# Optimization experiments

Hardware: AMD Instinct MI355X
Metric: run time of the kernel (lower is better)

The kernel has to match this reference:

```python
import jax, jax.numpy as jnp
import numpy as np

N = 100_000      # nodes
E = 3_200_000    # edges (avg degree 32)
F = 16           # irrep feature channels
IR = 4           # (max_l+1)**2 with max_l = 1
DENOM = 32.0     # denominator init kwarg
EPS = 1e-9
INV_S3 = 1.0 / np.sqrt(3.0).astype(np.float32)  # CG norm for 1x1->0
INV_S2 = 1.0 / np.sqrt(2.0).astype(np.float32)  # CG norm for 1x1->1


def setup_inputs() -> dict:
    key = jax.random.key(0)
    k0, k1, k2, k3, k4 = jax.random.split(key, 5)
    positions = jax.random.normal(k0, (N, 3), jnp.float32)
    node_feats = jax.random.normal(k1, (N, F, IR), jnp.float32)
    W = jax.random.normal(k2, (IR, IR), jnp.float32) / np.float32(np.sqrt(IR))
    b = jnp.zeros((IR,), jnp.float32)
    senders = jax.random.randint(k3, (E,), 0, N)
    receivers = jax.random.randint(k4, (E,), 0, N)
    return dict(positions=positions, node_feats=node_feats, W=W, b=b,
                senders=senders, receivers=receivers)


def reference(positions, node_feats, W, b, senders, receivers):
    # --- edge update: SH of normalized relative position, CG tensor product ---
    d = positions[receivers] - positions[senders]               # [E, 3]
    d = d / (jnp.linalg.norm(d, axis=-1, keepdims=True) + EPS)  # unit direction
    # real spherical harmonics up to l=1: sh0 = 1, sh1 = unit direction
    sh1 = d[:, None, :]                                         # [E, 1, 3]

    x = node_feats[senders]                                     # [E, F, 4]
    x0 = x[..., 0:1]                                            # l=0 part [E,F,1]
    x1 = x[..., 1:4]                                            # l=1 part [E,F,3]

    # CG paths with l3 <= max_l = 1:
    #   0x0->0 (identity), 1x1->0 (dot / sqrt3)
    out0 = x0 + jnp.sum(x1 * sh1, axis=-1, keepdims=True) * INV_S3      # [E,F,1]
    #   0x1->1, 1x0->1 (identities), 1x1->1 (cross / sqrt2)
    cross = jnp.cross(x1, jnp.broadcast_to(sh1, x1.shape))
    out1 = x0 * sh1 + x1 + cross * INV_S2                               # [E,F,3]
    tp = jnp.concatenate([out0, out1], axis=-1)                         # [E,F,4]

    # --- node update: segment-sum over receivers, scale, Dense over coeff dim ---
    agg = jax.ops.segment_sum(tp, receivers, num_segments=positions.shape[0])
    agg = agg / DENOM                                                   # [N,F,4]
    return agg @ W + b                                                  # [N,F,4]
```

## Files before the change

### kernel.cpp

```cpp
#include <hip/hip_runtime.h>
#include <hip/hip_fp16.h>


#define F_DIM 16
#define BIN_SHIFT 6
#define BIN_NODES (1 << BIN_SHIFT)
#define HALF_NODES (BIN_NODES / 2)
#define CHUNK 8192
#define CAP_LDS 1408
#define MAXBINS 2048

__global__ void __launch_bounds__(256) pack_kernel(
    const float* __restrict__ pos, const float* __restrict__ nf,
    float4* __restrict__ posf4, uint2* __restrict__ nfh,
    int* __restrict__ binCur, int N, int nbins, int cap)
{
    int tid = blockIdx.x * blockDim.x + threadIdx.x;
    int total = N * F_DIM;
    if (tid < total) {
        float4 q = ((const float4*)nf)[tid];
        __half2 h01 = __floats2half2_rn(q.x, q.y);
        __half2 h23 = __floats2half2_rn(q.z, q.w);
        uint2 u;
        u.x = *reinterpret_cast<unsigned*>(&h01);
        u.y = *reinterpret_cast<unsigned*>(&h23);
        nfh[tid] = u;
    }
    if (tid < N)
        posf4[tid] = make_float4(pos[3*tid], pos[3*tid+1], pos[3*tid+2], 0.f);
    if (tid < nbins)
        binCur[tid] = tid * cap;
}

__global__ void __launch_bounds__(512) build_bins_kernel(
    const int* __restrict__ senders, const int* __restrict__ receivers,
    int* __restrict__ binCur, int* __restrict__ bins,
    int nbins, int cap, int E)
{
    __shared__ int hbase[MAXBINS];
    __shared__ int hrank[MAXBINS];
    int t = threadIdx.x;
    for (int i = t; i < nbins; i += 512) { hbase[i] = 0; hrank[i] = 0; }
    __syncthreads();

    int base = blockIdx.x * CHUNK;
    int end  = base + CHUNK; if (end > E) end = E;

    for (int e = base + t; e < end; e += 512)
        atomicAdd(&hbase[((unsigned)receivers[e]) >> BIN_SHIFT], 1);
    __syncthreads();

    for (int i = t; i < nbins; i += 512) {
        int c = hbase[i];
        hbase[i] = (c > 0) ? atomicAdd(&binCur[i], c) : 0;
    }
    __syncthreads();

    for (int e = base + t; e < end; e += 512) {
        int r = receivers[e];
        int s = senders[e];
        int bb = r >> BIN_SHIFT;
        int rank = atomicAdd(&hrank[bb], 1);
        int dest = hbase[bb] + rank;
        if (dest < (bb + 1) * cap)
            bins[dest] = (s << BIN_SHIFT) | (r & (BIN_NODES - 1));
    }
}

__device__ __forceinline__ float4 unpack_h4(uint2 u)
{
    __half2 h01 = *reinterpret_cast<__half2*>(&u.x);
    __half2 h23 = *reinterpret_cast<__half2*>(&u.y);
    float2 a = __half22float2(h01);
    float2 b = __half22float2(h23);
    return make_float4(a.x, a.y, b.x, b.y);
}

__device__ __forceinline__ void edge_acc_d(
    float dx, float dy, float dz, const float4& fx,
    float& a0, float& a1, float& a2, float& a3)
{
    const float INV_S3 = 0.5773502691896258f;
    const float INV_S2 = 0.7071067811865476f;
    float dot = fx.y*dx + fx.z*dy + fx.w*dz;
    a0 += fx.x + dot * INV_S3;
    float c0 = fx.z*dz - fx.w*dy;
    float c1 = fx.w*dx - fx.y*dz;
    float c2 = fx.y*dy - fx.z*dx;
    a1 += fx.x*dx + fx.y + c0 * INV_S2;
    a2 += fx.x*dy + fx.z + c1 * INV_S2;
    a3 += fx.x*dz + fx.w + c2 * INV_S2;
}

__global__ void __launch_bounds__(256) bin_gather_kernel(
    const float4* __restrict__ posf4,
    const uint2* __restrict__ nfh,
    const int* __restrict__ bins,
    const int* __restrict__ binCur,
    const float* __restrict__ W,
    const float* __restrict__ Bias,
    float* __restrict__ out,
    int N, int cap)
{
    __shared__ float4 ledge[CAP_LDS];
    __shared__ int lhist[HALF_NODES];
    __shared__ int lscan[HALF_NODES];
    __shared__ int lstart[HALF_NODES];

    int t = threadIdx.x;
    int bin  = blockIdx.x >> 1;
    int half = blockIdx.x & 1;
    int node0 = (bin << BIN_SHIFT) + half * HALF_NODES;
    int gbase = bin * cap;

    int cnt = binCur[bin] - gbase;
    if (cnt > cap) cnt = cap;

    if (t < HALF_NODES) lhist[t] = 0;
    __syncthreads();

    for (int j = t; j < cnt; j += 256) {
        int rl = bins[gbase + j] & (BIN_NODES - 1);
        if ((rl >> 5) == half) atomicAdd(&lhist[rl & (HALF_NODES - 1)], 1);
    }
    __syncthreads();

    if (t < HALF_NODES) lscan[t] = lhist[t];
    __syncthreads();
    for (int off = 1; off < HALF_NODES; off <<= 1) {
        int v = (t < HALF_NODES && t >= off) ? lscan[t - off] : 0;
        __syncthreads();
        if (t < HALF_NODES) lscan[t] += v;
        __syncthreads();
    }
    if (t < HALF_NODES) { lstart[t] = lscan[t] - lhist[t]; lhist[t] = 0; }
    __syncthreads();

    for (int j = t; j < cnt; j += 256) {
        int pk = bins[gbase + j];
        int rl = pk & (BIN_NODES - 1);
        if ((rl >> 5) != half) continue;
        int rl32 = rl & (HALF_NODES - 1);
        int s = pk >> BIN_SHIFT;
        int rank = atomicAdd(&lhist[rl32], 1);
        int dest = lstart[rl32] + rank;
        if (dest >= CAP_LDS) continue;
        float4 ps = posf4[s];
        float4 pr = posf4[node0 + rl32];
        float dx = pr.x - ps.x;
        float dy = pr.y - ps.y;
        float dz = pr.z - ps.z;
        float d2 = dx*dx + dy*dy + dz*dz;
        float inv = __builtin_amdgcn_rsqf(fmaxf(d2, 1e-18f));
        float4 rec;
        rec.x = dx * inv;
        rec.y = dy * inv;
        rec.z = dz * inv;
        rec.w = __int_as_float(s);
        ledge[dest] = rec;
    }
    __syncthreads();

    float w[16];
#pragma unroll
    for (int i = 0; i < 16; ++i) w[i] = W[i];
    float b0 = Bias[0], b1 = Bias[1], b2 = Bias[2], b3 = Bias[3];
    const float sc = 1.0f / 32.0f;

    int f = t & 15;

    for (int nl = t >> 4; nl < HALF_NODES; nl += 16) {
        int n = node0 + nl;
        if (n >= N) break;
        int s0 = lstart[nl];
        int dcnt = lscan[nl] - s0;
        if (dcnt > CAP_LDS - s0) dcnt = CAP_LDS - s0;

        float a0 = 0.f, a1 = 0.f, a2 = 0.f, a3 = 0.f;
        int j = 0;
        for (; j + 4 <= dcnt; j += 4) {
            float4 e0 = ledge[s0 + j + 0];
            float4 e1 = ledge[s0 + j + 1];
            float4 e2 = ledge[s0 + j + 2];
            float4 e3 = ledge[s0 + j + 3];
            int s_0 = __float_as_int(e0.w);
            int s_1 = __float_as_int(e1.w);
            int s_2 = __float_as_int(e2.w);
            int s_3 = __float_as_int(e3.w);
            uint2 u0 = nfh[(unsigned)(s_0 * F_DIM + f)];
            uint2 u1 = nfh[(unsigned)(s_1 * F_DIM + f)];
            uint2 u2 = nfh[(unsigned)(s_2 * F_DIM + f)];
            uint2 u3 = nfh[(unsigned)(s_3 * F_DIM + f)];
            edge_acc_d(e0.x, e0.y, e0.z, unpack_h4(u0), a0, a1, a2, a3);
            edge_acc_d(e1.x, e1.y, e1.z, unpack_h4(u1), a0, a1, a2, a3);
            edge_acc_d(e2.x, e2.y, e2.z, unpack_h4(u2), a0, a1, a2, a3);
            edge_acc_d(e3.x, e3.y, e3.z, unpack_h4(u3), a0, a1, a2, a3);
        }
        for (; j < dcnt; ++j) {
            float4 e0 = ledge[s0 + j];
            int s = __float_as_int(e0.w);
            uint2 u = nfh[(unsigned)(s * F_DIM + f)];
            edge_acc_d(e0.x, e0.y, e0.z, unpack_h4(u), a0, a1, a2, a3);
        }

        a0 *= sc; a1 *= sc; a2 *= sc; a3 *= sc;
        float4 o;
        o.x = a0*w[0] + a1*w[4] + a2*w[8]  + a3*w[12] + b0;
        o.y = a0*w[1] + a1*w[5] + a2*w[9]  + a3*w[13] + b1;
        o.z = a0*w[2] + a1*w[6] + a2*w[10] + a3*w[14] + b2;
        o.w = a0*w[3] + a1*w[7] + a2*w[11] + a3*w[15] + b3;
        ((float4*)out)[(size_t)n * F_DIM + f] = o;
    }
}

__global__ void __launch_bounds__(256) hist_kernel(
    const int* __restrict__ receivers, int* __restrict__ deg,
    int* __restrict__ rank, int E)
{
    int e = blockIdx.x * blockDim.x + threadIdx.x;
    if (e >= E) return;
    rank[e] = atomicAdd(&deg[receivers[e]], 1);
}

__global__ void __launch_bounds__(256) alloc_kernel(
    const int* __restrict__ deg, int* __restrict__ start,
    int* __restrict__ cursor, int N)
{
    __shared__ int tmp[256];
    __shared__ int base;
    int t = threadIdx.x;
    int n = blockIdx.x * blockDim.x + t;
    int v = (n < N) ? deg[n] : 0;
    tmp[t] = v;
    __syncthreads();
    for (int off = 1; off < 256; off <<= 1) {
        int x = (t >= off) ? tmp[t - off] : 0;
        __syncthreads();
        tmp[t] += x;
        __syncthreads();
    }
    int incl = tmp[t];
    if (t == 255) base = atomicAdd(cursor, incl);
    __syncthreads();
    if (n < N) start[n] = base + incl - v;
}

__global__ void __launch_bounds__(256) scatter_kernel(
    const int* __restrict__ senders, const int* __restrict__ receivers,
    const int* __restrict__ rank, const int* __restrict__ start,
    int* __restrict__ csr_s, int E)
{
    int e = blockIdx.x * blockDim.x + threadIdx.x;
    if (e >= E) return;
    csr_s[start[receivers[e]] + rank[e]] = senders[e];
}

__global__ void __launch_bounds__(256) gather_kernel(
    const float* __restrict__ pos,
    const float* __restrict__ nf,
    const int* __restrict__ csr_s,
    const int* __restrict__ start,
    const int* __restrict__ deg,
    const float* __restrict__ W,
    const float* __restrict__ b,
    float* __restrict__ out,
    int N)
{
    const float INV_S3 = 0.5773502691896258f;
    const float INV_S2 = 0.7071067811865476f;

    int tid = blockIdx.x * blockDim.x + threadIdx.x;
    int n = tid >> 4;
    if (n >= N) return;
    int f = tid & 15;

    float rx = pos[3*n], ry = pos[3*n+1], rz = pos[3*n+2];
    int s0 = start[n];
    int dcnt = deg[n];
    float a0 = 0.f, a1 = 0.f, a2 = 0.f, a3 = 0.f;
    const float4* nf4 = (const float4*)nf;

    for (int j = 0; j < dcnt; ++j) {
        int s = csr_s[s0 + j];
        float dx = rx - pos[3*s], dy = ry - pos[3*s+1], dz = rz - pos[3*s+2];
        float d2 = dx*dx + dy*dy + dz*dz;
        float inv = __builtin_amdgcn_rsqf(fmaxf(d2, 1e-18f));
        dx *= inv; dy *= inv; dz *= inv;
        float4 x = nf4[(unsigned)(s * F_DIM + f)];
        float dot = x.y*dx + x.z*dy + x.w*dz;
        a0 += x.x + dot * INV_S3;
        float c0 = x.z*dz - x.w*dy, c1 = x.w*dx - x.y*dz, c2 = x.y*dy - x.z*dx;
        a1 += x.x*dx + x.y + c0 * INV_S2;
        a2 += x.x*dy + x.z + c1 * INV_S2;
        a3 += x.x*dz + x.w + c2 * INV_S2;
    }
    const float sc = 1.0f / 32.0f;
    a0 *= sc; a1 *= sc; a2 *= sc; a3 *= sc;
    float4 o;
    o.x = a0*W[0] + a1*W[4] + a2*W[8]  + a3*W[12] + b[0];
    o.y = a0*W[1] + a1*W[5] + a2*W[9]  + a3*W[13] + b[1];
    o.z = a0*W[2] + a1*W[6] + a2*W[10] + a3*W[14] + b[2];
    o.w = a0*W[3] + a1*W[7] + a2*W[11] + a3*W[15] + b[3];
    ((float4*)out)[tid] = o;
}

extern "C" void kernel_launch(void* const* d_in, const int* in_sizes, int n_in,
                              void* d_out, int out_size, void* d_ws, size_t ws_size,
                              hipStream_t stream)
{
    const float* pos       = (const float*)d_in[0];
    const float* nf        = (const float*)d_in[1];
    const float* W         = (const float*)d_in[2];
    const float* b         = (const float*)d_in[3];
    const int*   senders   = (const int*)d_in[4];
    const int*   receivers = (const int*)d_in[5];

    int N = in_sizes[0] / 3;
    int E = in_sizes[4];
    float* out = (float*)d_out;
    const int blk = 256;

    int nbins = (N + BIN_NODES - 1) >> BIN_SHIFT;
    int cap   = E / nbins + 453;
    size_t need = (size_t)N * 16 + (size_t)N * F_DIM * 8
                + ((size_t)nbins + (size_t)nbins * cap) * 4;

    if (nbins <= MAXBINS && ws_size >= need) {
        float4* posf4 = (float4*)d_ws;
        uint2*  nfh   = (uint2*)(posf4 + N);
        int* binCur = (int*)(nfh + (size_t)N * F_DIM);
        int* bins   = binCur + nbins;

        int total = N * F_DIM;
        pack_kernel<<<(total + blk - 1) / blk, blk, 0, stream>>>(
            pos, nf, posf4, nfh, binCur, N, nbins, cap);
        build_bins_kernel<<<(E + CHUNK - 1) / CHUNK, 512, 0, stream>>>(
            senders, receivers, binCur, bins, nbins, cap, E);
        bin_gather_kernel<<<nbins * 2, blk, 0, stream>>>(
            posf4, nfh, bins, binCur, W, b, out, N, cap);
    } else {
        int* cursor = (int*)d_ws;
        int* deg    = cursor + 1;
        int* start  = deg + N;
        int* rank   = start + N;
        int* csr_s  = rank + E;

        hipMemsetAsync(cursor, 0, (size_t)(1 + N) * sizeof(int), stream);
        hist_kernel<<<(E + blk - 1) / blk, blk, 0, stream>>>(receivers, deg, rank, E);
        alloc_kernel<<<(N + blk - 1) / blk, blk, 0, stream>>>(deg, start, cursor, N);
        scatter_kernel<<<(E + blk - 1) / blk, blk, 0, stream>>>(
            senders, receivers, rank, start, csr_s, E);
        long total = (long)N * F_DIM;
        gather_kernel<<<(unsigned)((total + blk - 1) / blk), blk, 0, stream>>>(
            pos, nf, csr_s, start, deg, W, b, out, N);
    }
}
```

Measured before the change: 239.7 us.

## Fuse feature packing into bin-building kernel and halve edge chunk size

Merges the separate pack kernel (fp16 conversion of node features, float4 positions) into the bin-building kernel with grid-stride loops, and replaces the bin-cursor initialisation with a memset so bin counters start at zero and are offset per bin. The chunk size drops from 8192 to 4096 edges and the block size from 512 to 256 threads, giving about twice as many blocks for the binning pass. This removes one kernel launch and its tail, at the cost of an added memset and more global atomics on bin counters from the larger block count.

```diff
diff --git a/kernel.cpp b/kernel.cpp
--- a/kernel.cpp
+++ b/kernel.cpp
@@ -6,66 +6,9 @@
 #define BIN_SHIFT 6
 #define BIN_NODES (1 << BIN_SHIFT)
 #define HALF_NODES (BIN_NODES / 2)
-#define CHUNK 8192
+#define CHUNK 4096
 #define CAP_LDS 1408
 #define MAXBINS 2048
-
-__global__ void __launch_bounds__(256) pack_kernel(
-    const float* __restrict__ pos, const float* __restrict__ nf,
-    float4* __restrict__ posf4, uint2* __restrict__ nfh,
-    int* __restrict__ binCur, int N, int nbins, int cap)
-{
-    int tid = blockIdx.x * blockDim.x + threadIdx.x;
-    int total = N * F_DIM;
-    if (tid < total) {
-        float4 q = ((const float4*)nf)[tid];
-        __half2 h01 = __floats2half2_rn(q.x, q.y);
-        __half2 h23 = __floats2half2_rn(q.z, q.w);
-        uint2 u;
-        u.x = *reinterpret_cast<unsigned*>(&h01);
-        u.y = *reinterpret_cast<unsigned*>(&h23);
-        nfh[tid] = u;
-    }
-    if (tid < N)
-        posf4[tid] = make_float4(pos[3*tid], pos[3*tid+1], pos[3*tid+2], 0.f);
-    if (tid < nbins)
-        binCur[tid] = tid * cap;
-}
-
-__global__ void __launch_bounds__(512) build_bins_kernel(
-    const int* __restrict__ senders, const int* __restrict__ receivers,
-    int* __restrict__ binCur, int* __restrict__ bins,
-    int nbins, int cap, int E)
-{
-    __shared__ int hbase[MAXBINS];
-    __shared__ int hrank[MAXBINS];
-    int t = threadIdx.x;
-    for (int i = t; i < nbins; i += 512) { hbase[i] = 0; hrank[i] = 0; }
-    __syncthreads();
-
-    int base = blockIdx.x * CHUNK;
-    int end  = base + CHUNK; if (end > E) end = E;
-
-    for (int e = base + t; e < end; e += 512)
-        atomicAdd(&hbase[((unsigned)receivers[e]) >> BIN_SHIFT], 1);
-    __syncthreads();
-
-    for (int i = t; i < nbins; i += 512) {
-        int c = hbase[i];
-        hbase[i] = (c > 0) ? atomicAdd(&binCur[i], c) : 0;
-    }
-    __syncthreads();
-
-    for (int e = base + t; e < end; e += 512) {
-        int r = receivers[e];
-        int s = senders[e];
-        int bb = r >> BIN_SHIFT;
-        int rank = atomicAdd(&hrank[bb], 1);
-        int dest = hbase[bb] + rank;
-        if (dest < (bb + 1) * cap)
-            bins[dest] = (s << BIN_SHIFT) | (r & (BIN_NODES - 1));
-    }
-}
 
 __device__ __forceinline__ float4 unpack_h4(uint2 u)
 {
@@ -92,6 +35,59 @@
     a3 += fx.x*dz + fx.w + c2 * INV_S2;
 }
 
+__global__ void __launch_bounds__(256) build_pack_kernel(
+    const float* __restrict__ pos, const float* __restrict__ nf,
+    const int* __restrict__ senders, const int* __restrict__ receivers,
+    float4* __restrict__ posf4, uint2* __restrict__ nfh,
+    int* __restrict__ binCur, int* __restrict__ bins,
+    int N, int E, int nbins, int cap)
+{
+    __shared__ int hbase[MAXBINS];
+    __shared__ int hrank[MAXBINS];
+    int t = threadIdx.x;
+    for (int i = t; i < nbins; i += 256) { hbase[i] = 0; hrank[i] = 0; }
+
+    int gtid = blockIdx.x * 256 + t;
+    int gstride = gridDim.x * 256;
+    int total = N * F_DIM;
+    for (int i = gtid; i < total; i += gstride) {
+        float4 q = ((const float4*)nf)[i];
+        __half2 h01 = __floats2half2_rn(q.x, q.y);
+        __half2 h23 = __floats2half2_rn(q.z, q.w);
+        uint2 u;
+        u.x = *reinterpret_cast<unsigned*>(&h01);
+        u.y = *reinterpret_cast<unsigned*>(&h23);
+        nfh[i] = u;
+    }
+    for (int i = gtid; i < N; i += gstride)
+        posf4[i] = make_float4(pos[3*i], pos[3*i+1], pos[3*i+2], 0.f);
+    __syncthreads();
+
+    int base = blockIdx.x * CHUNK;
+    int end  = base + CHUNK; if (end > E) end = E;
+    if (base >= end) return;
+
+    for (int e = base + t; e < end; e += 256)
+        atomicAdd(&hbase[((unsigned)receivers[e]) >> BIN_SHIFT], 1);
+    __syncthreads();
+
+    for (int i = t; i < nbins; i += 256) {
+        int c = hbase[i];
+        hbase[i] = (c > 0) ? atomicAdd(&binCur[i], c) : 0;
+    }
+    __syncthreads();
+
+    for (int e = base + t; e < end; e += 256) {
+        int r = receivers[e];
+        int s = senders[e];
+        int bb = r >> BIN_SHIFT;
+        int rank = atomicAdd(&hrank[bb], 1);
+        int dest = hbase[bb] + rank;
+        if (dest < cap)
+            bins[(size_t)bb * cap + dest] = (s << BIN_SHIFT) | (r & (BIN_NODES - 1));
+    }
+}
+
 __global__ void __launch_bounds__(256) bin_gather_kernel(
     const float4* __restrict__ posf4,
     const uint2* __restrict__ nfh,
@@ -113,7 +109,7 @@
     int node0 = (bin << BIN_SHIFT) + half * HALF_NODES;
     int gbase = bin * cap;
 
-    int cnt = binCur[bin] - gbase;
+    int cnt = binCur[bin];
     if (cnt > cap) cnt = cap;
 
     if (t < HALF_NODES) lhist[t] = 0;
@@ -331,11 +327,10 @@
         int* binCur = (int*)(nfh + (size_t)N * F_DIM);
         int* bins   = binCur + nbins;
 
-        int total = N * F_DIM;
-        pack_kernel<<<(total + blk - 1) / blk, blk, 0, stream>>>(
-            pos, nf, posf4, nfh, binCur, N, nbins, cap);
-        build_bins_kernel<<<(E + CHUNK - 1) / CHUNK, 512, 0, stream>>>(
-            senders, receivers, binCur, bins, nbins, cap, E);
+        hipMemsetAsync(binCur, 0, (size_t)nbins * sizeof(int), stream);
+        build_pack_kernel<<<(E + CHUNK - 1) / CHUNK, blk, 0, stream>>>(
+            pos, nf, senders, receivers, posf4, nfh, binCur, bins,
+            N, E, nbins, cap);
         bin_gather_kernel<<<nbins * 2, blk, 0, stream>>>(
             posf4, nfh, bins, binCur, W, b, out, N, cap);
     } else {
```

Measured after the change: 266.7 us. +11.2%, slower.

## Replace LDS-histogram binning with direct global atomics on padded bin counters

Applied to the files above, without the earlier changes.

Drops the two-pass block-local histogram and per-block reservation in the edge binning kernel. Instead, every edge does one global atomicAdd on a per-bin counter, with counters padded to 16 ints apart to avoid false sharing, and writes straight to its slot. This removes two LDS passes, the block syncs and the double read of receivers. The cost is 3.2M global atomics contending on about 1563 counters, and the order of edges within a bin is no longer deterministic.

```diff
diff --git a/kernel.cpp b/kernel.cpp
--- a/kernel.cpp
+++ b/kernel.cpp
@@ -6,14 +6,39 @@
 #define BIN_SHIFT 6
 #define BIN_NODES (1 << BIN_SHIFT)
 #define HALF_NODES (BIN_NODES / 2)
-#define CHUNK 8192
 #define CAP_LDS 1408
 #define MAXBINS 2048
+#define CUR_STRIDE 16
+
+__device__ __forceinline__ float4 unpack_h4(uint2 u)
+{
+    __half2 h01 = *reinterpret_cast<__half2*>(&u.x);
+    __half2 h23 = *reinterpret_cast<__half2*>(&u.y);
+    float2 a = __half22float2(h01);
+    float2 b = __half22float2(h23);
+    return make_float4(a.x, a.y, b.x, b.y);
+}
+
+__device__ __forceinline__ void edge_acc_d(
+    float dx, float dy, float dz, const float4& fx,
+    float& a0, float& a1, float& a2, float& a3)
+{
+    const float INV_S3 = 0.5773502691896258f;
+    const float INV_S2 = 0.7071067811865476f;
+    float dot = fx.y*dx + fx.z*dy + fx.w*dz;
+    a0 += fx.x + dot * INV_S3;
+    float c0 = fx.z*dz - fx.w*dy;
+    float c1 = fx.w*dx - fx.y*dz;
+    float c2 = fx.y*dy - fx.z*dx;
+    a1 += fx.x*dx + fx.y + c0 * INV_S2;
+    a2 += fx.x*dy + fx.z + c1 * INV_S2;
+    a3 += fx.x*dz + fx.w + c2 * INV_S2;
+}
 
 __global__ void __launch_bounds__(256) pack_kernel(
     const float* __restrict__ pos, const float* __restrict__ nf,
     float4* __restrict__ posf4, uint2* __restrict__ nfh,
-    int* __restrict__ binCur, int N, int nbins, int cap)
+    int* __restrict__ binCur, int N, int nbins)
 {
     int tid = blockIdx.x * blockDim.x + threadIdx.x;
     int total = N * F_DIM;
@@ -28,68 +53,25 @@
     }
     if (tid < N)
         posf4[tid] = make_float4(pos[3*tid], pos[3*tid+1], pos[3*tid+2], 0.f);
-    if (tid < nbins)
-        binCur[tid] = tid * cap;
-}
-
-__global__ void __launch_bounds__(512) build_bins_kernel(
+    if (tid < nbins * CUR_STRIDE)
+        binCur[tid] = 0;
+}
+
+__global__ void __launch_bounds__(256) build_kernel(
     const int* __restrict__ senders, const int* __restrict__ receivers,
     int* __restrict__ binCur, int* __restrict__ bins,
-    int nbins, int cap, int E)
-{
-    __shared__ int hbase[MAXBINS];
-    __shared__ int hrank[MAXBINS];
-    int t = threadIdx.x;
-    for (int i = t; i < nbins; i += 512) { hbase[i] = 0; hrank[i] = 0; }
-    __syncthreads();
-
-    int base = blockIdx.x * CHUNK;
-    int end  = base + CHUNK; if (end > E) end = E;
-
-    for (int e = base + t; e < end; e += 512)
-        atomicAdd(&hbase[((unsigned)receivers[e]) >> BIN_SHIFT], 1);
-    __syncthreads();
-
-    for (int i = t; i < nbins; i += 512) {
-        int c = hbase[i];
-        hbase[i] = (c > 0) ? atomicAdd(&binCur[i], c) : 0;
-    }
-    __syncthreads();
-
-    for (int e = base + t; e < end; e += 512) {
+    int cap, int E)
+{
+    int gtid = blockIdx.x * 256 + threadIdx.x;
+    int gstride = gridDim.x * 256;
+    for (int e = gtid; e < E; e += gstride) {
         int r = receivers[e];
         int s = senders[e];
         int bb = r >> BIN_SHIFT;
-        int rank = atomicAdd(&hrank[bb], 1);
-        int dest = hbase[bb] + rank;
-        if (dest < (bb + 1) * cap)
-            bins[dest] = (s << BIN_SHIFT) | (r & (BIN_NODES - 1));
-    }
-}
-
-__device__ __forceinline__ float4 unpack_h4(uint2 u)
-{
-    __half2 h01 = *reinterpret_cast<__half2*>(&u.x);
-    __half2 h23 = *reinterpret_cast<__half2*>(&u.y);
-    float2 a = __half22float2(h01);
-    float2 b = __half22float2(h23);
-    return make_float4(a.x, a.y, b.x, b.y);
-}
-
-__device__ __forceinline__ void edge_acc_d(
-    float dx, float dy, float dz, const float4& fx,
-    float& a0, float& a1, float& a2, float& a3)
-{
-    const float INV_S3 = 0.5773502691896258f;
-    const float INV_S2 = 0.7071067811865476f;
-    float dot = fx.y*dx + fx.z*dy + fx.w*dz;
-    a0 += fx.x + dot * INV_S3;
-    float c0 = fx.z*dz - fx.w*dy;
-    float c1 = fx.w*dx - fx.y*dz;
-    float c2 = fx.y*dy - fx.z*dx;
-    a1 += fx.x*dx + fx.y + c0 * INV_S2;
-    a2 += fx.x*dy + fx.z + c1 * INV_S2;
-    a3 += fx.x*dz + fx.w + c2 * INV_S2;
+        int rank = atomicAdd(&binCur[bb * CUR_STRIDE], 1);
+        if (rank < cap)
+            bins[(size_t)bb * cap + rank] = (s << BIN_SHIFT) | (r & (BIN_NODES - 1));
+    }
 }
 
 __global__ void __launch_bounds__(256) bin_gather_kernel(
@@ -113,7 +95,7 @@
     int node0 = (bin << BIN_SHIFT) + half * HALF_NODES;
     int gbase = bin * cap;
 
-    int cnt = binCur[bin] - gbase;
+    int cnt = binCur[bin * CUR_STRIDE];
     if (cnt > cap) cnt = cap;
 
     if (t < HALF_NODES) lhist[t] = 0;
@@ -323,19 +305,19 @@
     int nbins = (N + BIN_NODES - 1) >> BIN_SHIFT;
     int cap   = E / nbins + 453;
     size_t need = (size_t)N * 16 + (size_t)N * F_DIM * 8
-                + ((size_t)nbins + (size_t)nbins * cap) * 4;
+                + ((size_t)nbins * CUR_STRIDE + (size_t)nbins * cap) * 4;
 
     if (nbins <= MAXBINS && ws_size >= need) {
         float4* posf4 = (float4*)d_ws;
         uint2*  nfh   = (uint2*)(posf4 + N);
         int* binCur = (int*)(nfh + (size_t)N * F_DIM);
-        int* bins   = binCur + nbins;
+        int* bins   = binCur + (size_t)nbins * CUR_STRIDE;
 
         int total = N * F_DIM;
         pack_kernel<<<(total + blk - 1) / blk, blk, 0, stream>>>(
-            pos, nf, posf4, nfh, binCur, N, nbins, cap);
-        build_bins_kernel<<<(E + CHUNK - 1) / CHUNK, 512, 0, stream>>>(
-            senders, receivers, binCur, bins, nbins, cap, E);
+            pos, nf, posf4, nfh, binCur, N, nbins);
+        build_kernel<<<2048, blk, 0, stream>>>(
+            senders, receivers, binCur, bins, cap, E);
         bin_gather_kernel<<<nbins * 2, blk, 0, stream>>>(
             posf4, nfh, bins, binCur, W, b, out, N, cap);
     } else {
```

Measured after the change: 380.4 us. +58.7%, slower.

## Split each bin across four gather blocks and cache receiver positions in LDS

Applied to the files above, without the earlier changes.

The gather kernel now launches four blocks per 64-node bin, each handling 16 receivers, instead of two blocks handling 32. Each thread then owns exactly one node-feature pair, the per-block LDS edge buffer shrinks, and receiver positions are staged in shared memory. Bin cursors become relative counts, and the bin-building kernel uses 1024 threads per block. The aim is more blocks and higher occupancy for the gather phase, at the cost of every block rescanning the whole bin's edge list, now four times per bin instead of two.

```diff
diff --git a/kernel.cpp b/kernel.cpp
--- a/kernel.cpp
+++ b/kernel.cpp
@@ -5,15 +5,40 @@
 #define F_DIM 16
 #define BIN_SHIFT 6
 #define BIN_NODES (1 << BIN_SHIFT)
-#define HALF_NODES (BIN_NODES / 2)
+#define Q_NODES 16
 #define CHUNK 8192
-#define CAP_LDS 1408
+#define CAP_LDS 768
 #define MAXBINS 2048
+
+__device__ __forceinline__ float4 unpack_h4(uint2 u)
+{
+    __half2 h01 = *reinterpret_cast<__half2*>(&u.x);
+    __half2 h23 = *reinterpret_cast<__half2*>(&u.y);
+    float2 a = __half22float2(h01);
+    float2 b = __half22float2(h23);
+    return make_float4(a.x, a.y, b.x, b.y);
+}
+
+__device__ __forceinline__ void edge_acc_d(
+    float dx, float dy, float dz, const float4& fx,
+    float& a0, float& a1, float& a2, float& a3)
+{
+    const float INV_S3 = 0.5773502691896258f;
+    const float INV_S2 = 0.7071067811865476f;
+    float dot = fx.y*dx + fx.z*dy + fx.w*dz;
+    a0 += fx.x + dot * INV_S3;
+    float c0 = fx.z*dz - fx.w*dy;
+    float c1 = fx.w*dx - fx.y*dz;
+    float c2 = fx.y*dy - fx.z*dx;
+    a1 += fx.x*dx + fx.y + c0 * INV_S2;
+    a2 += fx.x*dy + fx.z + c1 * INV_S2;
+    a3 += fx.x*dz + fx.w + c2 * INV_S2;
+}
 
 __global__ void __launch_bounds__(256) pack_kernel(
     const float* __restrict__ pos, const float* __restrict__ nf,
     float4* __restrict__ posf4, uint2* __restrict__ nfh,
-    int* __restrict__ binCur, int N, int nbins, int cap)
+    int* __restrict__ binCur, int N, int nbins)
 {
     int tid = blockIdx.x * blockDim.x + threadIdx.x;
     int total = N * F_DIM;
@@ -29,10 +54,10 @@
     if (tid < N)
         posf4[tid] = make_float4(pos[3*tid], pos[3*tid+1], pos[3*tid+2], 0.f);
     if (tid < nbins)
-        binCur[tid] = tid * cap;
-}
-
-__global__ void __launch_bounds__(512) build_bins_kernel(
+        binCur[tid] = 0;
+}
+
+__global__ void __launch_bounds__(1024) build_bins_kernel(
     const int* __restrict__ senders, const int* __restrict__ receivers,
     int* __restrict__ binCur, int* __restrict__ bins,
     int nbins, int cap, int E)
@@ -40,56 +65,32 @@
     __shared__ int hbase[MAXBINS];
     __shared__ int hrank[MAXBINS];
     int t = threadIdx.x;
-    for (int i = t; i < nbins; i += 512) { hbase[i] = 0; hrank[i] = 0; }
+    for (int i = t; i < nbins; i += 1024) { hbase[i] = 0; hrank[i] = 0; }
     __syncthreads();
 
     int base = blockIdx.x * CHUNK;
     int end  = base + CHUNK; if (end > E) end = E;
-
-    for (int e = base + t; e < end; e += 512)
+    if (base >= end) return;
+
+    for (int e = base + t; e < end; e += 1024)
         atomicAdd(&hbase[((unsigned)receivers[e]) >> BIN_SHIFT], 1);
     __syncthreads();
 
-    for (int i = t; i < nbins; i += 512) {
+    for (int i = t; i < nbins; i += 1024) {
         int c = hbase[i];
         hbase[i] = (c > 0) ? atomicAdd(&binCur[i], c) : 0;
     }
     __syncthreads();
 
-    for (int e = base + t; e < end; e += 512) {
+    for (int e = base + t; e < end; e += 1024) {
         int r = receivers[e];
         int s = senders[e];
         int bb = r >> BIN_SHIFT;
         int rank = atomicAdd(&hrank[bb], 1);
         int dest = hbase[bb] + rank;
-        if (dest < (bb + 1) * cap)
-            bins[dest] = (s << BIN_SHIFT) | (r & (BIN_NODES - 1));
-    }
-}
-
-__device__ __forceinline__ float4 unpack_h4(uint2 u)
-{
-    __half2 h01 = *reinterpret_cast<__half2*>(&u.x);
-    __half2 h23 = *reinterpret_cast<__half2*>(&u.y);
-    float2 a = __half22float2(h01);
-    float2 b = __half22float2(h23);
-    return make_float4(a.x, a.y, b.x, b.y);
-}
-
-__device__ __forceinline__ void edge_acc_d(
-    float dx, float dy, float dz, const float4& fx,
-    float& a0, float& a1, float& a2, float& a3)
-{
-    const float INV_S3 = 0.5773502691896258f;
-    const float INV_S2 = 0.7071067811865476f;
-    float dot = fx.y*dx + fx.z*dy + fx.w*dz;
-    a0 += fx.x + dot * INV_S3;
-    float c0 = fx.z*dz - fx.w*dy;
-    float c1 = fx.w*dx - fx.y*dz;
-    float c2 = fx.y*dy - fx.z*dx;
-    a1 += fx.x*dx + fx.y + c0 * INV_S2;
-    a2 += fx.x*dy + fx.z + c1 * INV_S2;
-    a3 += fx.x*dz + fx.w + c2 * INV_S2;
+        if (dest < cap)
+            bins[(size_t)bb * cap + dest] = (s << BIN_SHIFT) | (r & (BIN_NODES - 1));
+    }
 }
 
 __global__ void __launch_bounds__(256) bin_gather_kernel(
@@ -103,50 +104,55 @@
     int N, int cap)
 {
     __shared__ float4 ledge[CAP_LDS];
-    __shared__ int lhist[HALF_NODES];
-    __shared__ int lscan[HALF_NODES];
-    __shared__ int lstart[HALF_NODES];
+    __shared__ float4 lpos[Q_NODES];
+    __shared__ int lhist[Q_NODES];
+    __shared__ int lscan[Q_NODES];
+    __shared__ int lstart[Q_NODES];
 
     int t = threadIdx.x;
-    int bin  = blockIdx.x >> 1;
-    int half = blockIdx.x & 1;
-    int node0 = (bin << BIN_SHIFT) + half * HALF_NODES;
+    int bin  = blockIdx.x >> 2;
+    int quad = blockIdx.x & 3;
+    int node0 = (bin << BIN_SHIFT) + quad * Q_NODES;
     int gbase = bin * cap;
 
-    int cnt = binCur[bin] - gbase;
+    int cnt = binCur[bin];
     if (cnt > cap) cnt = cap;
 
-    if (t < HALF_NODES) lhist[t] = 0;
+    if (t < Q_NODES) {
+        lhist[t] = 0;
+        int n = node0 + t;
+        lpos[t] = (n < N) ? posf4[n] : make_float4(0.f, 0.f, 0.f, 0.f);
+    }
     __syncthreads();
 
     for (int j = t; j < cnt; j += 256) {
         int rl = bins[gbase + j] & (BIN_NODES - 1);
-        if ((rl >> 5) == half) atomicAdd(&lhist[rl & (HALF_NODES - 1)], 1);
-    }
-    __syncthreads();
-
-    if (t < HALF_NODES) lscan[t] = lhist[t];
-    __syncthreads();
-    for (int off = 1; off < HALF_NODES; off <<= 1) {
-        int v = (t < HALF_NODES && t >= off) ? lscan[t - off] : 0;
+        if ((rl >> 4) == quad) atomicAdd(&lhist[rl & (Q_NODES - 1)], 1);
+    }
+    __syncthreads();
+
+    if (t < Q_NODES) lscan[t] = lhist[t];
+    __syncthreads();
+    for (int off = 1; off < Q_NODES; off <<= 1) {
+        int v = (t < Q_NODES && t >= off) ? lscan[t - off] : 0;
         __syncthreads();
-        if (t < HALF_NODES) lscan[t] += v;
+        if (t < Q_NODES) lscan[t] += v;
         __syncthreads();
     }
-    if (t < HALF_NODES) { lstart[t] = lscan[t] - lhist[t]; lhist[t] = 0; }
+    if (t < Q_NODES) { lstart[t] = lscan[t] - lhist[t]; lhist[t] = 0; }
     __syncthreads();
 
     for (int j = t; j < cnt; j += 256) {
         int pk = bins[gbase + j];
         int rl = pk & (BIN_NODES - 1);
-        if ((rl >> 5) != half) continue;
-        int rl32 = rl & (HALF_NODES - 1);
+        if ((rl >> 4) != quad) continue;
+        int rl16 = rl & (Q_NODES - 1);
         int s = pk >> BIN_SHIFT;
-        int rank = atomicAdd(&lhist[rl32], 1);
-        int dest = lstart[rl32] + rank;
+        int rank = atomicAdd(&lhist[rl16], 1);
+        int dest = lstart[rl16] + rank;
         if (dest >= CAP_LDS) continue;
         float4 ps = posf4[s];
-        float4 pr = posf4[node0 + rl32];
+        float4 pr = lpos[rl16];
         float dx = pr.x - ps.x;
         float dy = pr.y - ps.y;
         float dz = pr.z - ps.z;
@@ -168,10 +174,10 @@
     const float sc = 1.0f / 32.0f;
 
     int f = t & 15;
-
-    for (int nl = t >> 4; nl < HALF_NODES; nl += 16) {
-        int n = node0 + nl;
-        if (n >= N) break;
+    int nl = t >> 4;
+    int n = node0 + nl;
+
+    if (n < N) {
         int s0 = lstart[nl];
         int dcnt = lscan[nl] - s0;
         if (dcnt > CAP_LDS - s0) dcnt = CAP_LDS - s0;
@@ -333,10 +339,10 @@
 
         int total = N * F_DIM;
         pack_kernel<<<(total + blk - 1) / blk, blk, 0, stream>>>(
-            pos, nf, posf4, nfh, binCur, N, nbins, cap);
-        build_bins_kernel<<<(E + CHUNK - 1) / CHUNK, 512, 0, stream>>>(
+            pos, nf, posf4, nfh, binCur, N, nbins);
+        build_bins_kernel<<<(E + CHUNK - 1) / CHUNK, 1024, 0, stream>>>(
             senders, receivers, binCur, bins, nbins, cap, E);
-        bin_gather_kernel<<<nbins * 2, blk, 0, stream>>>(
+        bin_gather_kernel<<<nbins * 4, blk, 0, stream>>>(
             posf4, nfh, bins, binCur, W, b, out, N, cap);
     } else {
         int* cursor = (int*)d_ws;
```

Measured after the change: 246.6 us. 1.03x slower.
